# Performance work log

Measured on AMD Instinct MI355X. Metric: run time of the kernel, lower is better.

The kernel has to match this reference:

```python
import jax, jax.numpy as jnp
import numpy as np
import math

H, DK, DV = 16, 64, 64
D = H * DK  # model_dimension = 1024
N = M = L = 2048


def setup_inputs() -> dict:
    key = jax.random.key(0)
    ks = jax.random.split(key, 12)
    s = 1.0 / math.sqrt(DK)  # keep softmax logits in a sane range
    return {
        "queries": jax.random.normal(ks[0], (N, DK), jnp.float32),
        "keys": jax.random.normal(ks[1], (M, DK), jnp.float32),
        "values": jax.random.normal(ks[2], (L, DV), jnp.float32),
        "Wq": jax.random.normal(ks[3], (H, DK, D), jnp.float32) * s,
        "bq": jax.random.normal(ks[4], (H, D), jnp.float32) * 0.02,
        "Wk": jax.random.normal(ks[5], (H, DK, D), jnp.float32) * s,
        "bk": jax.random.normal(ks[6], (H, D), jnp.float32) * 0.02,
        "Wv": jax.random.normal(ks[7], (H, DV, D), jnp.float32) * s,
        "bv": jax.random.normal(ks[8], (H, D), jnp.float32) * 0.02,
        "Wo": jax.random.normal(ks[9], (D, H * DV), jnp.float32) * (1.0 / math.sqrt(H * DV)),
        "bo": jax.random.normal(ks[10], (D,), jnp.float32) * 0.02,
    }


def reference(queries, keys, values, Wq, bq, Wk, bk, Wv, bv, Wo, bo):
    # Batched per-head projections (original loops over heads in Python).
    Qp = jnp.einsum("nk,hkd->hnd", queries, Wq) + bq[:, None, :]   # (H, N, D)
    Kp = jnp.einsum("mk,hkd->hmd", keys, Wk) + bk[:, None, :]      # (H, M, D)
    Vp = jnp.einsum("lv,hvd->hld", values, Wv) + bv[:, None, :]    # (H, M, D)
    scores = jnp.einsum("hnd,hmd->hnm", Qp, Kp) / math.sqrt(DK)
    attn = jax.nn.softmax(scores, axis=-1)
    heads_out = jnp.einsum("hnm,hmd->hnd", attn, Vp)               # (H, N, D)
    # torch.concat(heads, dim=0).sum(dim=0) == sum over heads AND rows -> (D,)
    pooled = heads_out.sum(axis=(0, 1)).reshape(1, D)
    return pooled @ Wo.T + bo  # (1, D)
```

## Files before the change

kernel.cpp:

```cpp
#include <hip/hip_runtime.h>


typedef __attribute__((ext_vector_type(4))) float floatx4;
typedef __attribute__((ext_vector_type(8))) short shortx8;

__device__ inline unsigned short f2bf(float f) {
    unsigned int u = __float_as_uint(f);
    u += 0x7FFFu + ((u >> 16) & 1u);
    return (unsigned short)(u >> 16);
}
__device__ inline float bf2f(unsigned short s) {
    return __uint_as_float(((unsigned int)s) << 16);
}

__global__ __launch_bounds__(256) void prep_kernel(
    const float* __restrict__ Wq, const float* __restrict__ Wk,
    const float* __restrict__ bq, const float* __restrict__ keys,
    const float* __restrict__ values,
    float* __restrict__ Apart, float* __restrict__ vhpart,
    unsigned short* __restrict__ Kb, unsigned short* __restrict__ VT,
    float* __restrict__ r_ws) {
    const int tid = threadIdx.x;
    const int bx = blockIdx.x;
    __shared__ __align__(16) unsigned char sm[36352];
    if (bx < 128) {
        const int g = bx >> 4, h = bx & 15;
        const int c0 = g * 128;
        unsigned short* wq = (unsigned short*)sm;
        unsigned short* wk = (unsigned short*)(sm + 17408);
        float* bqs = (float*)(sm + 34816);
        float* vred = (float*)(sm + 35328);
        {
            int row = tid >> 2, cs = (tid & 3) * 32;
            const float* wqp = Wq + (size_t)(h * 64 + row) * 1024 + c0 + cs;
            const float* wkp = Wk + (size_t)(h * 64 + row) * 1024 + c0 + cs;
            #pragma unroll
            for (int u = 0; u < 8; ++u) {
                float4 a = *(const float4*)&wqp[u * 4];
                float4 b = *(const float4*)&wkp[u * 4];
                *(ushort4*)&wq[row * 136 + cs + u * 4] =
                    (ushort4){f2bf(a.x), f2bf(a.y), f2bf(a.z), f2bf(a.w)};
                *(ushort4*)&wk[row * 136 + cs + u * 4] =
                    (ushort4){f2bf(b.x), f2bf(b.y), f2bf(b.z), f2bf(b.w)};
            }
            if (tid < 128) bqs[tid] = bq[h * 1024 + c0 + tid];
        }
        __syncthreads();
        const int w = tid >> 6, lane = tid & 63;
        const int ln = lane & 15, quad = lane >> 4;
        {
            const int j = tid & 63, half = tid >> 6;
            float accv = 0.f;
            #pragma unroll
            for (int u = 0; u < 32; ++u)
                accv += bf2f(wk[j * 136 + half * 32 + u]) * bqs[half * 32 + u];
            vred[half * 64 + j] = accv;
        }
        shortx8 af[4];
        #pragma unroll
        for (int kk = 0; kk < 4; ++kk)
            af[kk] = *(shortx8*)&wq[(w * 16 + ln) * 136 + kk * 32 + quad * 8];
        float* ap = Apart + (size_t)bx * 4096;
        #pragma unroll
        for (int cn = 0; cn < 4; ++cn) {
            floatx4 acc = {};
            #pragma unroll
            for (int kk = 0; kk < 4; ++kk) {
                shortx8 bf_ = *(shortx8*)&wk[(cn * 16 + ln) * 136 + kk * 32 + quad * 8];
                acc = __builtin_amdgcn_mfma_f32_16x16x32_bf16(af[kk], bf_, acc, 0, 0, 0);
            }
            #pragma unroll
            for (int r = 0; r < 4; ++r)
                ap[(w * 16 + quad * 4 + r) * 64 + cn * 16 + ln] = acc[r];
        }
        __syncthreads();
        if (tid < 64)
            vhpart[bx * 64 + tid] = vred[tid] + vred[64 + tid] +
                                    vred[128 + tid] + vred[192 + tid];
    } else if (bx < 144) {
        int bk = bx - 128;
        int base = (bk * 256 + tid) * 32;
        #pragma unroll
        for (int u = 0; u < 8; ++u) {
            float4 a = *(const float4*)&keys[base + u * 4];
            *(ushort4*)&Kb[base + u * 4] =
                (ushort4){f2bf(a.x), f2bf(a.y), f2bf(a.z), f2bf(a.w)};
        }
        if (tid < 64) r_ws[bk * 64 + tid] = 0.f;
    } else {
        int bb = bx - 144, m0 = bb * 64;
        unsigned short* vts = (unsigned short*)sm;
        #pragma unroll
        for (int it = 0; it < 4; ++it) {
            int gi = tid + it * 256;
            int m = gi >> 4, c4 = (gi & 15) * 4;
            float4 a = *(const float4*)&values[(size_t)(m0 + m) * 64 + c4];
            vts[(c4 + 0) * 72 + m] = f2bf(a.x);
            vts[(c4 + 1) * 72 + m] = f2bf(a.y);
            vts[(c4 + 2) * 72 + m] = f2bf(a.z);
            vts[(c4 + 3) * 72 + m] = f2bf(a.w);
        }
        __syncthreads();
        #pragma unroll
        for (int it = 0; it < 2; ++it) {
            int gi = tid + it * 256;
            int v = gi >> 3, seg = (gi & 7) * 8;
            *(shortx8*)&VT[v * 2048 + m0 + seg] = *(shortx8*)&vts[v * 72 + seg];
        }
    }
}

__global__ __launch_bounds__(256) void reduceA_kernel(
    const float* __restrict__ Apart, const float* __restrict__ vhpart,
    unsigned short* __restrict__ Atlg, float* __restrict__ vhg) {
    const int tid = threadIdx.x;
    const int h = blockIdx.x >> 2, uq = blockIdx.x & 3;
    #pragma unroll
    for (int uu = 0; uu < 4; ++uu) {
        int e = (uq * 4 + uu) * 256 + tid;
        float s = 0.f;
        #pragma unroll
        for (int g = 0; g < 8; ++g)
            s += Apart[g * 65536 + h * 4096 + e];
        Atlg[h * 4096 + (e & 63) * 64 + (e >> 6)] = f2bf(s);
    }
    if (uq == 0 && tid < 64) {
        float s = 0.f;
        #pragma unroll
        for (int g = 0; g < 8; ++g) s += vhpart[(g * 16 + h) * 64 + tid];
        vhg[h * 64 + tid] = s;
    }
}

#define QSCALE 0.18033688f
__global__ __launch_bounds__(256, 4) void flash_kernel(
    const float* __restrict__ queries, const unsigned short* __restrict__ Atlg,
    const float* __restrict__ vhg, const unsigned short* __restrict__ Kb,
    const unsigned short* __restrict__ VT, float* __restrict__ r_ws) {
    const int h = blockIdx.y;
    const int n0 = blockIdx.x * 32;
    const int tid = threadIdx.x;
    const int w = tid >> 6, lane = tid & 63;
    const int ln = lane & 15, quad = lane >> 4;
    const int cw = w;

    __shared__ __align__(16) unsigned char lds[24064];
    __shared__ float vhs[64];
    unsigned short* qstage = (unsigned short*)lds;
    unsigned short* Atl = (unsigned short*)(lds + 4608);
    unsigned short* qh  = (unsigned short*)(lds + 19456);
    unsigned short* Pw  = (unsigned short*)(lds + w * 4864);
    float* LSUM = (float*)lds;
    float* LINV = (float*)(lds + 512);
    float* Rred = (float*)(lds + 640);

    {
        int row = tid >> 3, c8 = (tid & 7) * 8;
        const float* qp = queries + (size_t)(n0 + row) * 64 + c8;
        float4 a = *(const float4*)qp;
        float4 b = *(const float4*)(qp + 4);
        *(ushort4*)&qstage[row * 72 + c8] =
            (ushort4){f2bf(a.x), f2bf(a.y), f2bf(a.z), f2bf(a.w)};
        *(ushort4*)&qstage[row * 72 + c8 + 4] =
            (ushort4){f2bf(b.x), f2bf(b.y), f2bf(b.z), f2bf(b.w)};
    }
    #pragma unroll
    for (int k = 0; k < 2; ++k) {
        int seg = tid * 2 + k, row = seg >> 3, off = (seg & 7) * 8;
        *(shortx8*)&Atl[row * 72 + off] =
            *(const shortx8*)&Atlg[h * 4096 + row * 64 + off];
    }
    if (tid < 64) vhs[tid] = vhg[h * 64 + tid];
    __syncthreads();

    {
        const int t = w & 1, cnb = (w >> 1) * 2;
        shortx8 qa[2];
        #pragma unroll
        for (int kk = 0; kk < 2; ++kk)
            qa[kk] = *(shortx8*)&qstage[(t * 16 + ln) * 72 + kk * 32 + quad * 8];
        #pragma unroll
        for (int i = 0; i < 2; ++i) {
            int cn = cnb + i;
            floatx4 acc = {};
            #pragma unroll
            for (int kk = 0; kk < 2; ++kk) {
                shortx8 bfr = *(shortx8*)&Atl[(cn * 16 + ln) * 72 + kk * 32 + quad * 8];
                acc = __builtin_amdgcn_mfma_f32_16x16x32_bf16(qa[kk], bfr, acc, 0, 0, 0);
            }
            #pragma unroll
            for (int r = 0; r < 4; ++r)
                qh[(t * 16 + quad * 4 + r) * 72 + cn * 16 + ln] =
                    f2bf((acc[r] + vhs[cn * 16 + ln]) * QSCALE);
        }
    }
    __syncthreads();

    shortx8 qf[2][2];
    #pragma unroll
    for (int t = 0; t < 2; ++t)
        #pragma unroll
        for (int kk = 0; kk < 2; ++kk)
            qf[t][kk] = *(shortx8*)&qh[(t * 16 + ln) * 72 + kk * 32 + quad * 8];

    const unsigned short* KbC = Kb + (size_t)(cw * 512) * 64;
    const unsigned short* VTC = VT + cw * 512;
    shortx8 pk[8], pv[8];
    #pragma unroll
    for (int cm = 0; cm < 4; ++cm)
        #pragma unroll
        for (int kk = 0; kk < 2; ++kk)
            pk[cm * 2 + kk] = *(const shortx8*)
                &KbC[(size_t)(cm * 16 + ln) * 64 + kk * 32 + quad * 8];

    floatx4 O0[4] = {}, O1[4] = {};
    float lacc0[4] = {}, lacc1[4] = {};

    for (int s = 0; s < 8; ++s) {
        {
            int mb = s * 64;
            #pragma unroll
            for (int cv = 0; cv < 4; ++cv)
                #pragma unroll
                for (int hf = 0; hf < 2; ++hf)
                    pv[cv * 2 + hf] = *(const shortx8*)
                        &VTC[(size_t)(cv * 16 + ln) * 2048 + mb + hf * 32 + quad * 8];
        }
        floatx4 S0[4], S1[4];
        #pragma unroll
        for (int cm = 0; cm < 4; ++cm) {
            floatx4 a0 = {}, a1 = {};
            a0 = __builtin_amdgcn_mfma_f32_16x16x32_bf16(qf[0][0], pk[cm * 2], a0, 0, 0, 0);
            a0 = __builtin_amdgcn_mfma_f32_16x16x32_bf16(qf[0][1], pk[cm * 2 + 1], a0, 0, 0, 0);
            a1 = __builtin_amdgcn_mfma_f32_16x16x32_bf16(qf[1][0], pk[cm * 2], a1, 0, 0, 0);
            a1 = __builtin_amdgcn_mfma_f32_16x16x32_bf16(qf[1][1], pk[cm * 2 + 1], a1, 0, 0, 0);
            S0[cm] = a0; S1[cm] = a1;
        }
        if (s < 7) {
            int mb = (s + 1) * 64;
            #pragma unroll
            for (int cm = 0; cm < 4; ++cm)
                #pragma unroll
                for (int kk = 0; kk < 2; ++kk)
                    pk[cm * 2 + kk] = *(const shortx8*)
                        &KbC[(size_t)(mb + cm * 16 + ln) * 64 + kk * 32 + quad * 8];
        }
        #pragma unroll
        for (int cm = 0; cm < 4; ++cm) {
            #pragma unroll
            for (int r = 0; r < 4; ++r) {
                float p0 = __builtin_amdgcn_exp2f(S0[cm][r]); lacc0[r] += p0;
                Pw[(quad * 4 + r) * 76 + cm * 16 + ln] = f2bf(p0);
                float p1 = __builtin_amdgcn_exp2f(S1[cm][r]); lacc1[r] += p1;
                Pw[(16 + quad * 4 + r) * 76 + cm * 16 + ln] = f2bf(p1);
            }
        }
        shortx8 pf[2][2];
        #pragma unroll
        for (int t = 0; t < 2; ++t)
            #pragma unroll
            for (int kk = 0; kk < 2; ++kk)
                pf[t][kk] = *(shortx8*)&Pw[(t * 16 + ln) * 76 + kk * 32 + quad * 8];
        #pragma unroll
        for (int cv = 0; cv < 4; ++cv) {
            O0[cv] = __builtin_amdgcn_mfma_f32_16x16x32_bf16(pf[0][0], pv[cv * 2], O0[cv], 0, 0, 0);
            O0[cv] = __builtin_amdgcn_mfma_f32_16x16x32_bf16(pf[0][1], pv[cv * 2 + 1], O0[cv], 0, 0, 0);
            O1[cv] = __builtin_amdgcn_mfma_f32_16x16x32_bf16(pf[1][0], pv[cv * 2], O1[cv], 0, 0, 0);
            O1[cv] = __builtin_amdgcn_mfma_f32_16x16x32_bf16(pf[1][1], pv[cv * 2 + 1], O1[cv], 0, 0, 0);
        }
    }

    float lr0[4], lr1[4];
    #pragma unroll
    for (int r = 0; r < 4; ++r) {
        float x0 = lacc0[r], x1 = lacc1[r];
        #pragma unroll
        for (int o = 1; o <= 8; o <<= 1) { x0 += __shfl_xor(x0, o); x1 += __shfl_xor(x1, o); }
        lr0[r] = x0; lr1[r] = x1;
    }
    __syncthreads();
    if (ln == 0) {
        #pragma unroll
        for (int r = 0; r < 4; ++r) {
            LSUM[w * 32 + quad * 4 + r] = lr0[r];
            LSUM[w * 32 + 16 + quad * 4 + r] = lr1[r];
        }
    }
    __syncthreads();
    if (tid < 32)
        LINV[tid] = 1.0f / (LSUM[tid] + LSUM[32 + tid] + LSUM[64 + tid] + LSUM[96 + tid]);
    __syncthreads();
    {
        float sacc[4];
        #pragma unroll
        for (int cv = 0; cv < 4; ++cv) {
            float s = 0.f;
            #pragma unroll
            for (int r = 0; r < 4; ++r) {
                s += O0[cv][r] * LINV[quad * 4 + r];
                s += O1[cv][r] * LINV[16 + quad * 4 + r];
            }
            s += __shfl_xor(s, 16);
            s += __shfl_xor(s, 32);
            sacc[cv] = s;
        }
        if (quad == 0) {
            #pragma unroll
            for (int cv = 0; cv < 4; ++cv)
                Rred[w * 64 + cv * 16 + ln] = sacc[cv];
        }
    }
    __syncthreads();
    if (tid < 64)
        atomicAdd(&r_ws[h * 64 + tid],
                  Rred[tid] + Rred[64 + tid] + Rred[128 + tid] + Rred[192 + tid]);
}

__global__ __launch_bounds__(256) void pool_kernel(
    const float* __restrict__ Wv, const float* __restrict__ bv,
    const float* __restrict__ r_ws, float* __restrict__ pooled) {
    const int tid = threadIdx.x;
    const int d0 = blockIdx.x * 16;
    const int d = tid & 15, hh = tid >> 4;
    __shared__ float red[16][17];
    float acc = bv[hh * 1024 + d0 + d] * 2048.0f;
    const float* rv = r_ws + hh * 64;
    const float* wp = Wv + (size_t)hh * 64 * 1024 + d0 + d;
    #pragma unroll 8
    for (int v = 0; v < 64; ++v) acc += rv[v] * wp[(size_t)v * 1024];
    red[hh][d] = acc;
    __syncthreads();
    if (tid < 16) {
        float s = 0.f;
        #pragma unroll
        for (int g = 0; g < 16; ++g) s += red[g][tid];
        pooled[d0 + tid] = s;
    }
}

__global__ __launch_bounds__(256) void out_kernel(
    const float* __restrict__ Wo, const float* __restrict__ bo,
    const float* __restrict__ pooled, float* __restrict__ out) {
    const int tid = threadIdx.x, w = tid >> 6, lane = tid & 63;
    const int dp = blockIdx.x * 4 + w;
    const float* wr = Wo + (size_t)dp * 1024 + lane * 16;
    const float* pp = pooled + lane * 16;
    float acc = 0.f;
    #pragma unroll
    for (int u = 0; u < 4; ++u) {
        float4 a = *(const float4*)&wr[u * 4];
        float4 p = *(const float4*)&pp[u * 4];
        acc += a.x * p.x + a.y * p.y + a.z * p.z + a.w * p.w;
    }
    #pragma unroll
    for (int o = 32; o > 0; o >>= 1) acc += __shfl_xor(acc, o);
    if (lane == 0) out[dp] = acc + bo[dp];
}

extern "C" void kernel_launch(void* const* d_in, const int* in_sizes, int n_in,
                              void* d_out, int out_size, void* d_ws, size_t ws_size,
                              hipStream_t stream) {
    const float* queries = (const float*)d_in[0];
    const float* keys    = (const float*)d_in[1];
    const float* values  = (const float*)d_in[2];
    const float* Wq      = (const float*)d_in[3];
    const float* bq      = (const float*)d_in[4];
    const float* Wk      = (const float*)d_in[5];
    const float* Wv      = (const float*)d_in[7];
    const float* bv      = (const float*)d_in[8];
    const float* Wo      = (const float*)d_in[9];
    const float* bo      = (const float*)d_in[10];
    float* out = (float*)d_out;

    float* Apart  = (float*)d_ws;
    float* vhpart = Apart + 524288;
    float* r_ws   = vhpart + 8192;
    float* pooled = r_ws + 1024;
    unsigned short* Kb = (unsigned short*)(pooled + 1024);
    unsigned short* VT = Kb + 131072;
    unsigned short* Atlg = VT + 131072;
    float* vhg = (float*)(Atlg + 65536);

    prep_kernel<<<176, 256, 0, stream>>>(Wq, Wk, bq, keys, values,
                                         Apart, vhpart, Kb, VT, r_ws);
    reduceA_kernel<<<64, 256, 0, stream>>>(Apart, vhpart, Atlg, vhg);
    flash_kernel<<<dim3(64, 16), 256, 0, stream>>>(queries, Atlg, vhg,
                                                   Kb, VT, r_ws);
    pool_kernel<<<64, 256, 0, stream>>>(Wv, bv, r_ws, pooled);
    out_kernel<<<256, 256, 0, stream>>>(Wo, bo, pooled, out);
}
```

Baseline: 165.6 us.

## Software-pipeline K/V loads with inline asm waits and staggered tile order

The K and V tile loads in the flash kernel become inline-asm global loads, each tracked by an explicit vmcnt wait. The next K tile is issued in the middle of the QK MFMAs and the next V tile right after the PV MFMAs, so loads overlap compute. The starting tile is rotated per block to spread memory traffic. The launch-bounds occupancy hint drops from 4 to 3 to give the extra in-flight registers room, which may reduce wave occupancy.

```diff
diff --git a/kernel.cpp b/kernel.cpp
--- a/kernel.cpp
+++ b/kernel.cpp
@@ -12,6 +12,13 @@
 __device__ inline float bf2f(unsigned short s) {
     return __uint_as_float(((unsigned int)s) << 16);
 }
+
+#define GLOAD(dst, p) \
+    asm volatile("global_load_dwordx4 %0, %1, off" : "=&v"(dst) : "v"(p))
+#define TIEDWAIT(cnt, a) \
+    asm volatile("s_waitcnt vmcnt(" #cnt ")" \
+        : "+v"(a[0]), "+v"(a[1]), "+v"(a[2]), "+v"(a[3]), \
+          "+v"(a[4]), "+v"(a[5]), "+v"(a[6]), "+v"(a[7]) :: "memory")
 
 __global__ __launch_bounds__(256) void prep_kernel(
     const float* __restrict__ Wq, const float* __restrict__ Wk,
@@ -133,7 +140,7 @@
 }
 
 #define QSCALE 0.18033688f
-__global__ __launch_bounds__(256, 4) void flash_kernel(
+__global__ __launch_bounds__(256, 3) void flash_kernel(
     const float* __restrict__ queries, const unsigned short* __restrict__ Atlg,
     const float* __restrict__ vhg, const unsigned short* __restrict__ Kb,
     const unsigned short* __restrict__ VT, float* __restrict__ r_ws) {
@@ -205,28 +212,28 @@
 
     const unsigned short* KbC = Kb + (size_t)(cw * 512) * 64;
     const unsigned short* VTC = VT + cw * 512;
+    const int boff = (blockIdx.x * 3 + h) & 7;
+
     shortx8 pk[8], pv[8];
-    #pragma unroll
-    for (int cm = 0; cm < 4; ++cm)
-        #pragma unroll
-        for (int kk = 0; kk < 2; ++kk)
-            pk[cm * 2 + kk] = *(const shortx8*)
-                &KbC[(size_t)(cm * 16 + ln) * 64 + kk * 32 + quad * 8];
+    {
+        const int s0 = boff;
+        #pragma unroll
+        for (int j = 0; j < 8; ++j)
+            GLOAD(pk[j], KbC + ((size_t)(s0 * 64 + (j >> 1) * 16 + ln) * 64 +
+                                (j & 1) * 32 + quad * 8));
+        #pragma unroll
+        for (int j = 0; j < 8; ++j)
+            GLOAD(pv[j], VTC + ((size_t)((j >> 1) * 16 + ln) * 2048 + s0 * 64 +
+                                (j & 1) * 32 + quad * 8));
+    }
 
     floatx4 O0[4] = {}, O1[4] = {};
     float lacc0[4] = {}, lacc1[4] = {};
 
-    for (int s = 0; s < 8; ++s) {
-        {
-            int mb = s * 64;
-            #pragma unroll
-            for (int cv = 0; cv < 4; ++cv)
-                #pragma unroll
-                for (int hf = 0; hf < 2; ++hf)
-                    pv[cv * 2 + hf] = *(const shortx8*)
-                        &VTC[(size_t)(cv * 16 + ln) * 2048 + mb + hf * 32 + quad * 8];
-        }
-        floatx4 S0[4], S1[4];
+    #pragma unroll
+    for (int i = 0; i < 8; ++i) {
+        const int sn = (i + 1 + boff) & 7;
+        TIEDWAIT(8, pk);
         #pragma unroll
         for (int cm = 0; cm < 4; ++cm) {
             floatx4 a0 = {}, a1 = {};
@@ -234,24 +241,17 @@
             a0 = __builtin_amdgcn_mfma_f32_16x16x32_bf16(qf[0][1], pk[cm * 2 + 1], a0, 0, 0, 0);
             a1 = __builtin_amdgcn_mfma_f32_16x16x32_bf16(qf[1][0], pk[cm * 2], a1, 0, 0, 0);
             a1 = __builtin_amdgcn_mfma_f32_16x16x32_bf16(qf[1][1], pk[cm * 2 + 1], a1, 0, 0, 0);
-            S0[cm] = a0; S1[cm] = a1;
-        }
-        if (s < 7) {
-            int mb = (s + 1) * 64;
-            #pragma unroll
-            for (int cm = 0; cm < 4; ++cm)
+            if (cm == 3 && i < 7) {
                 #pragma unroll
-                for (int kk = 0; kk < 2; ++kk)
-                    pk[cm * 2 + kk] = *(const shortx8*)
-                        &KbC[(size_t)(mb + cm * 16 + ln) * 64 + kk * 32 + quad * 8];
-        }
-        #pragma unroll
-        for (int cm = 0; cm < 4; ++cm) {
+                for (int j = 0; j < 8; ++j)
+                    GLOAD(pk[j], KbC + ((size_t)(sn * 64 + (j >> 1) * 16 + ln) * 64 +
+                                        (j & 1) * 32 + quad * 8));
+            }
             #pragma unroll
             for (int r = 0; r < 4; ++r) {
-                float p0 = __builtin_amdgcn_exp2f(S0[cm][r]); lacc0[r] += p0;
+                float p0 = __builtin_amdgcn_exp2f(a0[r]); lacc0[r] += p0;
                 Pw[(quad * 4 + r) * 76 + cm * 16 + ln] = f2bf(p0);
-                float p1 = __builtin_amdgcn_exp2f(S1[cm][r]); lacc1[r] += p1;
+                float p1 = __builtin_amdgcn_exp2f(a1[r]); lacc1[r] += p1;
                 Pw[(16 + quad * 4 + r) * 76 + cm * 16 + ln] = f2bf(p1);
             }
         }
@@ -261,12 +261,19 @@
             #pragma unroll
             for (int kk = 0; kk < 2; ++kk)
                 pf[t][kk] = *(shortx8*)&Pw[(t * 16 + ln) * 76 + kk * 32 + quad * 8];
+        if (i < 7) { TIEDWAIT(8, pv); } else { TIEDWAIT(0, pv); }
         #pragma unroll
         for (int cv = 0; cv < 4; ++cv) {
             O0[cv] = __builtin_amdgcn_mfma_f32_16x16x32_bf16(pf[0][0], pv[cv * 2], O0[cv], 0, 0, 0);
             O0[cv] = __builtin_amdgcn_mfma_f32_16x16x32_bf16(pf[0][1], pv[cv * 2 + 1], O0[cv], 0, 0, 0);
             O1[cv] = __builtin_amdgcn_mfma_f32_16x16x32_bf16(pf[1][0], pv[cv * 2], O1[cv], 0, 0, 0);
             O1[cv] = __builtin_amdgcn_mfma_f32_16x16x32_bf16(pf[1][1], pv[cv * 2 + 1], O1[cv], 0, 0, 0);
+        }
+        if (i < 7) {
+            #pragma unroll
+            for (int j = 0; j < 8; ++j)
+                GLOAD(pv[j], VTC + ((size_t)((j >> 1) * 16 + ln) * 2048 + sn * 64 +
+                                    (j & 1) * 32 + quad * 8));
         }
     }
 
```

Measured after the change: 201.8 us. 21.9% more time.

## Pre-swizzle K and V^T into MFMA fragment order for coalesced loads

Applied to the files above, without the earlier changes.

The prep kernel now writes the bf16 keys and transposed values in a fragment-major layout. Each wave's MFMA operand fragment then becomes one contiguous 1 KB chunk, so the flash kernel loads each operand as lane*8 plus j*512 instead of strided row gathers. This is meant to make global/L2 reads of K and V fully coalesced and to cut address arithmetic. The flash kernel's launch bound also drops from 4 to 3 blocks per SIMD, which gives more registers but may reduce occupancy.

```diff
diff --git a/kernel.cpp b/kernel.cpp
--- a/kernel.cpp
+++ b/kernel.cpp
@@ -18,7 +18,7 @@
     const float* __restrict__ bq, const float* __restrict__ keys,
     const float* __restrict__ values,
     float* __restrict__ Apart, float* __restrict__ vhpart,
-    unsigned short* __restrict__ Kb, unsigned short* __restrict__ VT,
+    unsigned short* __restrict__ KbS, unsigned short* __restrict__ VTS,
     float* __restrict__ r_ws) {
     const int tid = threadIdx.x;
     const int bx = blockIdx.x;
@@ -79,12 +79,18 @@
                                     vred[128 + tid] + vred[192 + tid];
     } else if (bx < 144) {
         int bk = bx - 128;
-        int base = (bk * 256 + tid) * 32;
-        #pragma unroll
-        for (int u = 0; u < 8; ++u) {
-            float4 a = *(const float4*)&keys[base + u * 4];
-            *(ushort4*)&Kb[base + u * 4] =
+        int m = bk * 128 + (tid >> 1), hf = tid & 1;
+        int b = m >> 6, cm = (m >> 4) & 3, ln = m & 15;
+        const float* kp = keys + (size_t)m * 64 + hf * 32;
+        unsigned short* dst = KbS + ((size_t)((b * 4 + cm) * 2 + hf) * 512 + ln * 8);
+        #pragma unroll
+        for (int q0 = 0; q0 < 4; ++q0) {
+            float4 a = *(const float4*)&kp[q0 * 8];
+            float4 c = *(const float4*)&kp[q0 * 8 + 4];
+            *(ushort4*)&dst[q0 * 128] =
                 (ushort4){f2bf(a.x), f2bf(a.y), f2bf(a.z), f2bf(a.w)};
+            *(ushort4*)&dst[q0 * 128 + 4] =
+                (ushort4){f2bf(c.x), f2bf(c.y), f2bf(c.z), f2bf(c.w)};
         }
         if (tid < 64) r_ws[bk * 64 + tid] = 0.f;
     } else {
@@ -104,8 +110,10 @@
         #pragma unroll
         for (int it = 0; it < 2; ++it) {
             int gi = tid + it * 256;
-            int v = gi >> 3, seg = (gi & 7) * 8;
-            *(shortx8*)&VT[v * 2048 + m0 + seg] = *(shortx8*)&vts[v * 72 + seg];
+            int v = gi >> 3, hf = (gi >> 2) & 1, quad = gi & 3;
+            *(shortx8*)&VTS[(size_t)((bb * 4 + (v >> 4)) * 2 + hf) * 512 +
+                            (quad * 16 + (v & 15)) * 8] =
+                *(shortx8*)&vts[v * 72 + hf * 32 + quad * 8];
         }
     }
 }
@@ -133,10 +141,10 @@
 }
 
 #define QSCALE 0.18033688f
-__global__ __launch_bounds__(256, 4) void flash_kernel(
+__global__ __launch_bounds__(256, 3) void flash_kernel(
     const float* __restrict__ queries, const unsigned short* __restrict__ Atlg,
-    const float* __restrict__ vhg, const unsigned short* __restrict__ Kb,
-    const unsigned short* __restrict__ VT, float* __restrict__ r_ws) {
+    const float* __restrict__ vhg, const unsigned short* __restrict__ KbS,
+    const unsigned short* __restrict__ VTS, float* __restrict__ r_ws) {
     const int h = blockIdx.y;
     const int n0 = blockIdx.x * 32;
     const int tid = threadIdx.x;
@@ -203,28 +211,23 @@
         for (int kk = 0; kk < 2; ++kk)
             qf[t][kk] = *(shortx8*)&qh[(t * 16 + ln) * 72 + kk * 32 + quad * 8];
 
-    const unsigned short* KbC = Kb + (size_t)(cw * 512) * 64;
-    const unsigned short* VTC = VT + cw * 512;
+    const unsigned short* KbC = KbS + (size_t)cw * 8 * 4096 + lane * 8;
+    const unsigned short* VTC = VTS + (size_t)cw * 8 * 4096 + lane * 8;
+
     shortx8 pk[8], pv[8];
     #pragma unroll
-    for (int cm = 0; cm < 4; ++cm)
-        #pragma unroll
-        for (int kk = 0; kk < 2; ++kk)
-            pk[cm * 2 + kk] = *(const shortx8*)
-                &KbC[(size_t)(cm * 16 + ln) * 64 + kk * 32 + quad * 8];
+    for (int j = 0; j < 8; ++j)
+        pk[j] = *(const shortx8*)&KbC[j * 512];
 
     floatx4 O0[4] = {}, O1[4] = {};
     float lacc0[4] = {}, lacc1[4] = {};
 
-    for (int s = 0; s < 8; ++s) {
+    for (int i = 0; i < 8; ++i) {
         {
-            int mb = s * 64;
-            #pragma unroll
-            for (int cv = 0; cv < 4; ++cv)
-                #pragma unroll
-                for (int hf = 0; hf < 2; ++hf)
-                    pv[cv * 2 + hf] = *(const shortx8*)
-                        &VTC[(size_t)(cv * 16 + ln) * 2048 + mb + hf * 32 + quad * 8];
+            const unsigned short* vb = VTC + (size_t)i * 4096;
+            #pragma unroll
+            for (int j = 0; j < 8; ++j)
+                pv[j] = *(const shortx8*)&vb[j * 512];
         }
         floatx4 S0[4], S1[4];
         #pragma unroll
@@ -236,14 +239,11 @@
             a1 = __builtin_amdgcn_mfma_f32_16x16x32_bf16(qf[1][1], pk[cm * 2 + 1], a1, 0, 0, 0);
             S0[cm] = a0; S1[cm] = a1;
         }
-        if (s < 7) {
-            int mb = (s + 1) * 64;
-            #pragma unroll
-            for (int cm = 0; cm < 4; ++cm)
-                #pragma unroll
-                for (int kk = 0; kk < 2; ++kk)
-                    pk[cm * 2 + kk] = *(const shortx8*)
-                        &KbC[(size_t)(mb + cm * 16 + ln) * 64 + kk * 32 + quad * 8];
+        if (i < 7) {
+            const unsigned short* kb = KbC + (size_t)(i + 1) * 4096;
+            #pragma unroll
+            for (int j = 0; j < 8; ++j)
+                pk[j] = *(const shortx8*)&kb[j * 512];
         }
         #pragma unroll
         for (int cm = 0; cm < 4; ++cm) {
@@ -376,16 +376,16 @@
     float* vhpart = Apart + 524288;
     float* r_ws   = vhpart + 8192;
     float* pooled = r_ws + 1024;
-    unsigned short* Kb = (unsigned short*)(pooled + 1024);
-    unsigned short* VT = Kb + 131072;
-    unsigned short* Atlg = VT + 131072;
+    unsigned short* KbS = (unsigned short*)(pooled + 1024);
+    unsigned short* VTS = KbS + 131072;
+    unsigned short* Atlg = VTS + 131072;
     float* vhg = (float*)(Atlg + 65536);
 
     prep_kernel<<<176, 256, 0, stream>>>(Wq, Wk, bq, keys, values,
-                                         Apart, vhpart, Kb, VT, r_ws);
+                                         Apart, vhpart, KbS, VTS, r_ws);
     reduceA_kernel<<<64, 256, 0, stream>>>(Apart, vhpart, Atlg, vhg);
     flash_kernel<<<dim3(64, 16), 256, 0, stream>>>(queries, Atlg, vhg,
-                                                   Kb, VT, r_ws);
+                                                   KbS, VTS, r_ws);
     pool_kernel<<<64, 256, 0, stream>>>(Wv, bv, r_ws, pooled);
     out_kernel<<<256, 256, 0, stream>>>(Wo, bo, pooled, out);
 }
```

Result: faster. 133.6 us (-19.3%).

## Restructure flash kernel to stream K/V through shared double-buffered LDS across 8 waves

Applied to the files above, without the earlier changes.

Each block now owns 128 query rows with 8 waves, one 16-row tile per wave. The waves iterate together over all 2048 keys, with K and V tiles staged cooperatively into double-buffered LDS. Previously each block held 32 rows with 4 waves, and each wave split the key range and loaded K/V fragments straight from global memory into registers. The change aims to cut redundant global K/V traffic by sharing tiles across more query rows and to simplify the final row-sum reduction. The cost is a barrier every iteration, larger LDS (about 72KB) and a smaller grid (256 blocks), which lowers occupancy and parallelism.

```diff
diff --git a/kernel.cpp b/kernel.cpp
--- a/kernel.cpp
+++ b/kernel.cpp
@@ -133,40 +133,38 @@
 }
 
 #define QSCALE 0.18033688f
-__global__ __launch_bounds__(256, 4) void flash_kernel(
+__global__ __launch_bounds__(512, 2) void flash_kernel(
     const float* __restrict__ queries, const unsigned short* __restrict__ Atlg,
     const float* __restrict__ vhg, const unsigned short* __restrict__ Kb,
     const unsigned short* __restrict__ VT, float* __restrict__ r_ws) {
     const int h = blockIdx.y;
-    const int n0 = blockIdx.x * 32;
+    const int n0 = blockIdx.x * 128;
     const int tid = threadIdx.x;
     const int w = tid >> 6, lane = tid & 63;
     const int ln = lane & 15, quad = lane >> 4;
-    const int cw = w;
-
-    __shared__ __align__(16) unsigned char lds[24064];
+
+    __shared__ __align__(16) unsigned char lds[73728];
     __shared__ float vhs[64];
+    unsigned short* Kbuf = (unsigned short*)lds;
+    unsigned short* Vbuf = (unsigned short*)(lds + 18432);
+    unsigned short* qh   = (unsigned short*)(lds + 36864);
+    unsigned short* Pw   = (unsigned short*)(lds + 55296 + w * 2304);
     unsigned short* qstage = (unsigned short*)lds;
-    unsigned short* Atl = (unsigned short*)(lds + 4608);
-    unsigned short* qh  = (unsigned short*)(lds + 19456);
-    unsigned short* Pw  = (unsigned short*)(lds + w * 4864);
-    float* LSUM = (float*)lds;
-    float* LINV = (float*)(lds + 512);
-    float* Rred = (float*)(lds + 640);
+    unsigned short* Atl  = (unsigned short*)(lds + 18432);
+    float* Rred = (float*)lds;
 
     {
-        int row = tid >> 3, c8 = (tid & 7) * 8;
-        const float* qp = queries + (size_t)(n0 + row) * 64 + c8;
-        float4 a = *(const float4*)qp;
-        float4 b = *(const float4*)(qp + 4);
-        *(ushort4*)&qstage[row * 72 + c8] =
-            (ushort4){f2bf(a.x), f2bf(a.y), f2bf(a.z), f2bf(a.w)};
-        *(ushort4*)&qstage[row * 72 + c8 + 4] =
-            (ushort4){f2bf(b.x), f2bf(b.y), f2bf(b.z), f2bf(b.w)};
-    }
-    #pragma unroll
-    for (int k = 0; k < 2; ++k) {
-        int seg = tid * 2 + k, row = seg >> 3, off = (seg & 7) * 8;
+        int row = tid >> 2, c16 = (tid & 3) * 16;
+        const float* qp = queries + (size_t)(n0 + row) * 64 + c16;
+        #pragma unroll
+        for (int u = 0; u < 4; ++u) {
+            float4 a = *(const float4*)&qp[u * 4];
+            *(ushort4*)&qstage[row * 72 + c16 + u * 4] =
+                (ushort4){f2bf(a.x), f2bf(a.y), f2bf(a.z), f2bf(a.w)};
+        }
+    }
+    {
+        int row = tid >> 3, off = (tid & 7) * 8;
         *(shortx8*)&Atl[row * 72 + off] =
             *(const shortx8*)&Atlg[h * 4096 + row * 64 + off];
     }
@@ -174,14 +172,12 @@
     __syncthreads();
 
     {
-        const int t = w & 1, cnb = (w >> 1) * 2;
         shortx8 qa[2];
         #pragma unroll
         for (int kk = 0; kk < 2; ++kk)
-            qa[kk] = *(shortx8*)&qstage[(t * 16 + ln) * 72 + kk * 32 + quad * 8];
-        #pragma unroll
-        for (int i = 0; i < 2; ++i) {
-            int cn = cnb + i;
+            qa[kk] = *(shortx8*)&qstage[(w * 16 + ln) * 72 + kk * 32 + quad * 8];
+        #pragma unroll
+        for (int cn = 0; cn < 4; ++cn) {
             floatx4 acc = {};
             #pragma unroll
             for (int kk = 0; kk < 2; ++kk) {
@@ -190,130 +186,108 @@
             }
             #pragma unroll
             for (int r = 0; r < 4; ++r)
-                qh[(t * 16 + quad * 4 + r) * 72 + cn * 16 + ln] =
+                qh[(w * 16 + quad * 4 + r) * 72 + cn * 16 + ln] =
                     f2bf((acc[r] + vhs[cn * 16 + ln]) * QSCALE);
         }
     }
     __syncthreads();
 
-    shortx8 qf[2][2];
-    #pragma unroll
-    for (int t = 0; t < 2; ++t)
+    const int srow = tid >> 3, scol = (tid & 7) * 8;
+    {
+        shortx8 kr = *(const shortx8*)&Kb[(size_t)srow * 64 + scol];
+        shortx8 vr = *(const shortx8*)&VT[srow * 2048 + scol];
+        *(shortx8*)&Kbuf[srow * 72 + scol] = kr;
+        *(shortx8*)&Vbuf[srow * 72 + scol] = vr;
+    }
+    shortx8 qf[2];
+    #pragma unroll
+    for (int kk = 0; kk < 2; ++kk)
+        qf[kk] = *(shortx8*)&qh[(w * 16 + ln) * 72 + kk * 32 + quad * 8];
+    __syncthreads();
+
+    floatx4 O[4] = {};
+    float lacc[4] = {};
+    for (int s = 0; s < 32; ++s) {
+        const int b = s & 1;
+        const unsigned short* kb = Kbuf + b * 4608;
+        const unsigned short* vb = Vbuf + b * 4608;
+        shortx8 krn, vrn;
+        if (s < 31) {
+            int m0n = (s + 1) * 64;
+            krn = *(const shortx8*)&Kb[(size_t)(m0n + srow) * 64 + scol];
+            vrn = *(const shortx8*)&VT[srow * 2048 + m0n + scol];
+        }
+        floatx4 S[4];
+        #pragma unroll
+        for (int cm = 0; cm < 4; ++cm) {
+            floatx4 acc = {};
+            #pragma unroll
+            for (int kk = 0; kk < 2; ++kk) {
+                shortx8 kf = *(const shortx8*)&kb[(cm * 16 + ln) * 72 + kk * 32 + quad * 8];
+                acc = __builtin_amdgcn_mfma_f32_16x16x32_bf16(qf[kk], kf, acc, 0, 0, 0);
+            }
+            S[cm] = acc;
+        }
+        #pragma unroll
+        for (int cm = 0; cm < 4; ++cm) {
+            #pragma unroll
+            for (int r = 0; r < 4; ++r) {
+                float p = __builtin_amdgcn_exp2f(S[cm][r]);
+                lacc[r] += p;
+                Pw[(quad * 4 + r) * 72 + cm * 16 + ln] = f2bf(p);
+            }
+        }
+        shortx8 pf[2];
         #pragma unroll
         for (int kk = 0; kk < 2; ++kk)
-            qf[t][kk] = *(shortx8*)&qh[(t * 16 + ln) * 72 + kk * 32 + quad * 8];
-
-    const unsigned short* KbC = Kb + (size_t)(cw * 512) * 64;
-    const unsigned short* VTC = VT + cw * 512;
-    shortx8 pk[8], pv[8];
-    #pragma unroll
-    for (int cm = 0; cm < 4; ++cm)
-        #pragma unroll
-        for (int kk = 0; kk < 2; ++kk)
-            pk[cm * 2 + kk] = *(const shortx8*)
-                &KbC[(size_t)(cm * 16 + ln) * 64 + kk * 32 + quad * 8];
-
-    floatx4 O0[4] = {}, O1[4] = {};
-    float lacc0[4] = {}, lacc1[4] = {};
-
-    for (int s = 0; s < 8; ++s) {
-        {
-            int mb = s * 64;
-            #pragma unroll
-            for (int cv = 0; cv < 4; ++cv)
-                #pragma unroll
-                for (int hf = 0; hf < 2; ++hf)
-                    pv[cv * 2 + hf] = *(const shortx8*)
-                        &VTC[(size_t)(cv * 16 + ln) * 2048 + mb + hf * 32 + quad * 8];
-        }
-        floatx4 S0[4], S1[4];
-        #pragma unroll
-        for (int cm = 0; cm < 4; ++cm) {
-            floatx4 a0 = {}, a1 = {};
-            a0 = __builtin_amdgcn_mfma_f32_16x16x32_bf16(qf[0][0], pk[cm * 2], a0, 0, 0, 0);
-            a0 = __builtin_amdgcn_mfma_f32_16x16x32_bf16(qf[0][1], pk[cm * 2 + 1], a0, 0, 0, 0);
-            a1 = __builtin_amdgcn_mfma_f32_16x16x32_bf16(qf[1][0], pk[cm * 2], a1, 0, 0, 0);
-            a1 = __builtin_amdgcn_mfma_f32_16x16x32_bf16(qf[1][1], pk[cm * 2 + 1], a1, 0, 0, 0);
-            S0[cm] = a0; S1[cm] = a1;
-        }
-        if (s < 7) {
-            int mb = (s + 1) * 64;
-            #pragma unroll
-            for (int cm = 0; cm < 4; ++cm)
-                #pragma unroll
-                for (int kk = 0; kk < 2; ++kk)
-                    pk[cm * 2 + kk] = *(const shortx8*)
-                        &KbC[(size_t)(mb + cm * 16 + ln) * 64 + kk * 32 + quad * 8];
-        }
-        #pragma unroll
-        for (int cm = 0; cm < 4; ++cm) {
-            #pragma unroll
-            for (int r = 0; r < 4; ++r) {
-                float p0 = __builtin_amdgcn_exp2f(S0[cm][r]); lacc0[r] += p0;
-                Pw[(quad * 4 + r) * 76 + cm * 16 + ln] = f2bf(p0);
-                float p1 = __builtin_amdgcn_exp2f(S1[cm][r]); lacc1[r] += p1;
-                Pw[(16 + quad * 4 + r) * 76 + cm * 16 + ln] = f2bf(p1);
-            }
-        }
-        shortx8 pf[2][2];
-        #pragma unroll
-        for (int t = 0; t < 2; ++t)
-            #pragma unroll
-            for (int kk = 0; kk < 2; ++kk)
-                pf[t][kk] = *(shortx8*)&Pw[(t * 16 + ln) * 76 + kk * 32 + quad * 8];
+            pf[kk] = *(shortx8*)&Pw[ln * 72 + kk * 32 + quad * 8];
         #pragma unroll
         for (int cv = 0; cv < 4; ++cv) {
-            O0[cv] = __builtin_amdgcn_mfma_f32_16x16x32_bf16(pf[0][0], pv[cv * 2], O0[cv], 0, 0, 0);
-            O0[cv] = __builtin_amdgcn_mfma_f32_16x16x32_bf16(pf[0][1], pv[cv * 2 + 1], O0[cv], 0, 0, 0);
-            O1[cv] = __builtin_amdgcn_mfma_f32_16x16x32_bf16(pf[1][0], pv[cv * 2], O1[cv], 0, 0, 0);
-            O1[cv] = __builtin_amdgcn_mfma_f32_16x16x32_bf16(pf[1][1], pv[cv * 2 + 1], O1[cv], 0, 0, 0);
-        }
-    }
-
-    float lr0[4], lr1[4];
+            shortx8 v0 = *(const shortx8*)&vb[(cv * 16 + ln) * 72 + quad * 8];
+            shortx8 v1 = *(const shortx8*)&vb[(cv * 16 + ln) * 72 + 32 + quad * 8];
+            O[cv] = __builtin_amdgcn_mfma_f32_16x16x32_bf16(pf[0], v0, O[cv], 0, 0, 0);
+            O[cv] = __builtin_amdgcn_mfma_f32_16x16x32_bf16(pf[1], v1, O[cv], 0, 0, 0);
+        }
+        if (s < 31) {
+            unsigned short* kbn = Kbuf + (b ^ 1) * 4608;
+            unsigned short* vbn = Vbuf + (b ^ 1) * 4608;
+            *(shortx8*)&kbn[srow * 72 + scol] = krn;
+            *(shortx8*)&vbn[srow * 72 + scol] = vrn;
+        }
+        __syncthreads();
+    }
+
+    float linv[4];
     #pragma unroll
     for (int r = 0; r < 4; ++r) {
-        float x0 = lacc0[r], x1 = lacc1[r];
-        #pragma unroll
-        for (int o = 1; o <= 8; o <<= 1) { x0 += __shfl_xor(x0, o); x1 += __shfl_xor(x1, o); }
-        lr0[r] = x0; lr1[r] = x1;
-    }
-    __syncthreads();
-    if (ln == 0) {
-        #pragma unroll
-        for (int r = 0; r < 4; ++r) {
-            LSUM[w * 32 + quad * 4 + r] = lr0[r];
-            LSUM[w * 32 + 16 + quad * 4 + r] = lr1[r];
-        }
-    }
-    __syncthreads();
-    if (tid < 32)
-        LINV[tid] = 1.0f / (LSUM[tid] + LSUM[32 + tid] + LSUM[64 + tid] + LSUM[96 + tid]);
-    __syncthreads();
-    {
-        float sacc[4];
-        #pragma unroll
-        for (int cv = 0; cv < 4; ++cv) {
-            float s = 0.f;
-            #pragma unroll
-            for (int r = 0; r < 4; ++r) {
-                s += O0[cv][r] * LINV[quad * 4 + r];
-                s += O1[cv][r] * LINV[16 + quad * 4 + r];
-            }
-            s += __shfl_xor(s, 16);
-            s += __shfl_xor(s, 32);
-            sacc[cv] = s;
-        }
-        if (quad == 0) {
-            #pragma unroll
-            for (int cv = 0; cv < 4; ++cv)
-                Rred[w * 64 + cv * 16 + ln] = sacc[cv];
-        }
-    }
-    __syncthreads();
-    if (tid < 64)
-        atomicAdd(&r_ws[h * 64 + tid],
-                  Rred[tid] + Rred[64 + tid] + Rred[128 + tid] + Rred[192 + tid]);
+        float x = lacc[r];
+        #pragma unroll
+        for (int o = 1; o <= 8; o <<= 1) x += __shfl_xor(x, o);
+        linv[r] = 1.0f / x;
+    }
+    float sacc[4];
+    #pragma unroll
+    for (int cv = 0; cv < 4; ++cv) {
+        float s = 0.f;
+        #pragma unroll
+        for (int r = 0; r < 4; ++r) s += O[cv][r] * linv[r];
+        s += __shfl_xor(s, 16);
+        s += __shfl_xor(s, 32);
+        sacc[cv] = s;
+    }
+    __syncthreads();
+    if (quad == 0) {
+        #pragma unroll
+        for (int cv = 0; cv < 4; ++cv)
+            Rred[w * 64 + cv * 16 + ln] = sacc[cv];
+    }
+    __syncthreads();
+    if (tid < 64) {
+        float s = 0.f;
+        #pragma unroll
+        for (int g = 0; g < 8; ++g) s += Rred[g * 64 + tid];
+        atomicAdd(&r_ws[h * 64 + tid], s);
+    }
 }
 
 __global__ __launch_bounds__(256) void pool_kernel(
@@ -384,7 +358,7 @@
     prep_kernel<<<176, 256, 0, stream>>>(Wq, Wk, bq, keys, values,
                                          Apart, vhpart, Kb, VT, r_ws);
     reduceA_kernel<<<64, 256, 0, stream>>>(Apart, vhpart, Atlg, vhg);
-    flash_kernel<<<dim3(64, 16), 256, 0, stream>>>(queries, Atlg, vhg,
+    flash_kernel<<<dim3(16, 16), 512, 0, stream>>>(queries, Atlg, vhg,
                                                    Kb, VT, r_ws);
     pool_kernel<<<64, 256, 0, stream>>>(Wv, bv, r_ws, pooled);
     out_kernel<<<256, 256, 0, stream>>>(Wo, bo, pooled, out);
```

Result: faster. 132.6 us (-19.9%).
